# Performance work log

Hardware: AMD Instinct MI355X
Metric: run time of the kernel (lower is better)

## Reference

```python
import jax, jax.numpy as jnp
import numpy as np

N_HEADS = 32
N_KV_HEADS = 8
HEAD_DIM = 128  # hidden 4096 / 32
NEG_INF = -1e9


def _apply_rope(x, cos, sin):
    # x: [B, S, H, D]; cos/sin: [S, D//2] -> complex multiply on (even, odd) pairs
    B, S, H, D = x.shape
    xr = x.reshape(B, S, H, D // 2, 2)
    a, b = xr[..., 0], xr[..., 1]
    c = cos[None, :, None, :]
    s = sin[None, :, None, :]
    out = jnp.stack([a * c - b * s, a * s + b * c], axis=-1)
    return out.reshape(B, S, H, D)


def setup_inputs() -> dict:
    key = jax.random.key(0)
    ks = jax.random.split(key, 8)
    B, S, HID = 1, 2048, 4096
    hidden_states = jax.random.normal(ks[0], (B, S, HID), dtype=jnp.float32)
    # causal additive mask [1,1,S,S]
    causal = jnp.tril(jnp.ones((S, S), dtype=bool))
    attention_mask = jnp.where(causal, 0.0, NEG_INF).astype(jnp.float32)[None, None]
    # true rotary frequencies (theta=500000 as in llama3)
    half = HEAD_DIM // 2
    inv_freq = 1.0 / (500000.0 ** (np.arange(0, half, dtype=np.float32) / half))
    angles = np.arange(S, dtype=np.float32)[:, None] * inv_freq[None, :]
    freqs_cos = jnp.asarray(np.cos(angles), dtype=jnp.float32)
    freqs_sin = jnp.asarray(np.sin(angles), dtype=jnp.float32)
    sc = 0.02
    wq = jax.random.normal(ks[1], (HID, HID), dtype=jnp.float32) * sc
    wk = jax.random.normal(ks[2], (N_KV_HEADS * HEAD_DIM, HID), dtype=jnp.float32) * sc
    wv = jax.random.normal(ks[3], (N_KV_HEADS * HEAD_DIM, HID), dtype=jnp.float32) * sc
    wo = jax.random.normal(ks[4], (HID, HID), dtype=jnp.float32) * sc
    return {"hidden_states": hidden_states, "attention_mask": attention_mask,
            "freqs_cos": freqs_cos, "freqs_sin": freqs_sin,
            "wq": wq, "wk": wk, "wv": wv, "wo": wo}


def reference(hidden_states, attention_mask, freqs_cos, freqs_sin, wq, wk, wv, wo):
    B, S, HID = hidden_states.shape
    n_rep = N_HEADS // N_KV_HEADS
    # projections (torch Linear: x @ W.T)
    q = (hidden_states @ wq.T).reshape(B, S, N_HEADS, HEAD_DIM)
    k = (hidden_states @ wk.T).reshape(B, S, N_KV_HEADS, HEAD_DIM)
    v = (hidden_states @ wv.T).reshape(B, S, N_KV_HEADS, HEAD_DIM)
    # rotary on q (full cos/sin) and k
    q = _apply_rope(q, freqs_cos, freqs_sin)
    k = _apply_rope(k, freqs_cos, freqs_sin)
    # [B, H, S, D]
    q = q.transpose(0, 2, 1, 3)
    k = k.transpose(0, 2, 1, 3)
    v = v.transpose(0, 2, 1, 3)
    # GQA: repeat_interleave kv heads
    k = jnp.repeat(k, n_rep, axis=1)
    v = jnp.repeat(v, n_rep, axis=1)
    scores = jnp.einsum("bhqd,bhkd->bhqk", q, k) / jnp.sqrt(jnp.float32(HEAD_DIM))
    scores = scores + attention_mask
    probs = jax.nn.softmax(scores.astype(jnp.float32), axis=-1)
    attn = jnp.einsum("bhqk,bhkd->bhqd", probs, v)
    attn = attn.transpose(0, 2, 1, 3).reshape(B, S, N_HEADS * HEAD_DIM)
    return attn @ wo.T
```

## Files before the change

### kernel.cpp

```cpp
#include <hip/hip_runtime.h>
#include <hip/hip_bf16.h>
#include <math.h>

#define SEQ 2048
#define HID 4096
#define NH 32
#define NKV 8
#define HD 128
#define KVG (NH / NKV)
#define NQKV 6144

typedef __bf16 bf16x8 __attribute__((ext_vector_type(8)));
typedef float  f32x4  __attribute__((ext_vector_type(4)));

__device__ __forceinline__ unsigned short f2bf(float f) {
  union { float f; unsigned int u; } v; v.f = f;
  unsigned int r = v.u + 0x7FFFu + ((v.u >> 16) & 1u);
  return (unsigned short)(r >> 16);
}
__device__ __forceinline__ float bf2f(unsigned short h) {
  union { unsigned int u; float f; } v; v.u = ((unsigned int)h) << 16;
  return v.f;
}

__device__ __forceinline__ void glds16(const unsigned short* g, unsigned short* l) {
  __builtin_amdgcn_global_load_lds(
      (const __attribute__((address_space(1))) void*)g,
      (__attribute__((address_space(3))) void*)l, 16, 0, 0);
}

__global__ __launch_bounds__(256) void cvt_all(
    const float* __restrict__ H, const float* __restrict__ wq,
    const float* __restrict__ wk, const float* __restrict__ wv,
    const float* __restrict__ wo, unsigned short* __restrict__ ws)
{
  const long G1 = 1l << 20;
  const long M1 = 1l << 20;
  long g = (long)blockIdx.x * 256 + threadIdx.x;
  const float* src; unsigned short* dst; long rel;
  if      (g < 2 * G1) { src = H;  dst = ws;           rel = g;          }
  else if (g < 6 * G1) { src = wq; dst = ws + 8 * M1;  rel = g - 2 * G1; }
  else if (g < 7 * G1) { src = wk; dst = ws + 24 * M1; rel = g - 6 * G1; }
  else if (g < 8 * G1) { src = wv; dst = ws + 28 * M1; rel = g - 7 * G1; }
  else                 { src = wo; dst = ws + 32 * M1; rel = g - 8 * G1; }
  float4 v = ((const float4*)src)[rel];
  ushort4 o;
  o.x = f2bf(v.x); o.y = f2bf(v.y); o.z = f2bf(v.z); o.w = f2bf(v.w);
  ((ushort4*)dst)[rel] = o;
}

template<bool F32OUT>
__global__ __launch_bounds__(256) void gemm_nt(
    const unsigned short* __restrict__ A,
    const unsigned short* __restrict__ B,
    void* __restrict__ Cv,
    int M, int N, int K)
{
  __shared__ unsigned short As[128 * 64];
  __shared__ unsigned short Bs[128 * 64];
  const int t = threadIdx.x;
  const int lane = t & 63, wid = t >> 6;
  const int quad = lane >> 4, l16 = lane & 15;
  const int wm = (wid & 1) * 64, wn = (wid >> 1) * 64;
  const int m0 = blockIdx.y * 128, n0 = blockIdx.x * 128;

  int srow[4], sgch[4];
  const unsigned short* ga[4];
  const unsigned short* gb[4];
  unsigned short* la[4];
  unsigned short* lb[4];
  #pragma unroll
  for (int j = 0; j < 4; j++) {
    int pj = (wid * 4 + j) * 64 + lane;
    srow[j] = pj >> 3;
    sgch[j] = (pj & 7) ^ (srow[j] & 7);
    ga[j] = A + (size_t)(m0 + srow[j]) * K + sgch[j] * 8;
    gb[j] = B + (size_t)(n0 + srow[j]) * K + sgch[j] * 8;
    la[j] = &As[(wid * 4 + j) * 512];
    lb[j] = &Bs[(wid * 4 + j) * 512];
  }

  const f32x4 fzero = {0.f, 0.f, 0.f, 0.f};
  f32x4 acc[4][4];
  #pragma unroll
  for (int i = 0; i < 4; i++)
    #pragma unroll
    for (int j = 0; j < 4; j++) acc[i][j] = fzero;

  for (int k0 = 0; k0 < K; k0 += 64) {
    __syncthreads();
    #pragma unroll
    for (int j = 0; j < 4; j++) {
      glds16(ga[j], la[j]);
      glds16(gb[j], lb[j]);
      ga[j] += 64; gb[j] += 64;
    }
    __syncthreads();

    #pragma unroll
    for (int ks = 0; ks < 2; ks++) {
      bf16x8 af[4], bfr[4];
      #pragma unroll
      for (int mt = 0; mt < 4; mt++) {
        int row = wm + mt * 16 + l16;
        int cp = (ks * 4 + quad) ^ (l16 & 7);
        af[mt] = *(const bf16x8*)(&As[(row * 8 + cp) * 8]);
      }
      #pragma unroll
      for (int nt = 0; nt < 4; nt++) {
        int row = wn + nt * 16 + l16;
        int cp = (ks * 4 + quad) ^ (l16 & 7);
        bfr[nt] = *(const bf16x8*)(&Bs[(row * 8 + cp) * 8]);
      }
      #pragma unroll
      for (int mt = 0; mt < 4; mt++)
        #pragma unroll
        for (int nt = 0; nt < 4; nt++)
          acc[mt][nt] = __builtin_amdgcn_mfma_f32_16x16x32_bf16(af[mt], bfr[nt], acc[mt][nt], 0, 0, 0);
    }
  }

  #pragma unroll
  for (int mt = 0; mt < 4; mt++)
    #pragma unroll
    for (int nt = 0; nt < 4; nt++)
      #pragma unroll
      for (int r = 0; r < 4; r++) {
        int row = m0 + wm + mt * 16 + quad * 4 + r;
        int col = n0 + wn + nt * 16 + l16;
        float v = acc[mt][nt][r];
        if (F32OUT) ((float*)Cv)[(size_t)row * N + col] = v;
        else        ((unsigned short*)Cv)[(size_t)row * N + col] = f2bf(v);
      }
}

__global__ __launch_bounds__(256) void rope_vtrans(
    const unsigned short* __restrict__ QKVr,
    const float* __restrict__ cosT,
    const float* __restrict__ sinT,
    unsigned short* __restrict__ Qh,
    unsigned short* __restrict__ Kh,
    unsigned short* __restrict__ Vtg)
{
  __shared__ unsigned short T[64 * 66];
  int hh = blockIdx.y;
  int bx = blockIdx.x;
  int t = threadIdx.x;
  if (hh < NH + NKV) {
    int sub = t >> 6, d2 = t & 63;
    int s = bx * 4 + sub;
    float c = cosT[s * 64 + d2], sn = sinT[s * 64 + d2];
    const unsigned short* src;
    unsigned short* dst;
    if (hh < NH) {
      src = QKVr + (size_t)s * NQKV + hh * HD;
      dst = Qh + ((size_t)hh * SEQ + s) * HD;
    } else {
      int h = hh - NH;
      src = QKVr + (size_t)s * NQKV + HID + h * HD;
      dst = Kh + ((size_t)h * SEQ + s) * HD;
    }
    unsigned int u = *(const unsigned int*)(src + 2 * d2);
    float a = bf2f((unsigned short)(u & 0xffff)), b = bf2f((unsigned short)(u >> 16));
    unsigned int o = (unsigned int)f2bf(a * c - b * sn) | ((unsigned int)f2bf(a * sn + b * c) << 16);
    *(unsigned int*)(dst + 2 * d2) = o;
  } else {
    int idx = bx >> 5;
    int kvh = idx >> 1, d0 = (idx & 1) * 64;
    int s0 = (bx & 31) * 64;
    int si = t >> 2, dchunk = t & 3;
    const unsigned short* src = QKVr + (size_t)(s0 + si) * NQKV + HID + NKV * HD + kvh * HD + d0 + dchunk * 16;
    uint4 a = *(const uint4*)src;
    uint4 b = *(const uint4*)(src + 8);
    unsigned int va[8] = {a.x, a.y, a.z, a.w, b.x, b.y, b.z, b.w};
    #pragma unroll
    for (int j = 0; j < 8; j++)
      *(unsigned int*)(&T[si * 66 + dchunk * 16 + j * 2]) = va[j];
    __syncthreads();
    int di = t >> 2, schunk = t & 3;
    unsigned short px[16];
    #pragma unroll
    for (int j = 0; j < 16; j++) px[j] = T[(schunk * 16 + j) * 66 + di];
    unsigned short* dst = Vtg + ((size_t)kvh * HD + d0 + di) * SEQ + s0 + schunk * 16;
    *(uint4*)dst = *(uint4*)px;
    *(uint4*)(dst + 8) = *(uint4*)(px + 8);
  }
}

__global__ __launch_bounds__(256) void flash_kernel(
    const unsigned short* __restrict__ Qh,
    const unsigned short* __restrict__ Kh,
    const unsigned short* __restrict__ Vtg,
    unsigned short* __restrict__ Obf)
{
  __shared__ unsigned short Ks[64 * 128];
  __shared__ unsigned short Vs[128 * 64];
  __shared__ unsigned short Ps[4][32 * 72];

  const int h = blockIdx.y;
  const int pairp = blockIdx.x;
  const int kvh = h / KVG;
  const int t = threadIdx.x;
  const int lane = t & 63, w = t >> 6;
  const int quad = lane >> 4, l16 = lane & 15;
  const float scale = 0.08838834764831845f;
  const float SHIFT = 8.0f;

  bf16x8 ones;
  #pragma unroll
  for (int j = 0; j < 8; j++) ones[j] = (__bf16)1.0f;

  int krow[4], kgch[4], vrow[4], vgch[4];
  unsigned short* lk[4];
  unsigned short* lv[4];
  #pragma unroll
  for (int j = 0; j < 4; j++) {
    int pj = (w * 4 + j) * 64 + lane;
    krow[j] = pj >> 4; kgch[j] = (pj & 15) ^ (krow[j] & 15);
    vrow[j] = pj >> 3; vgch[j] = (pj & 7) ^ (vrow[j] & 7);
    lk[j] = &Ks[(w * 4 + j) * 512];
    lv[j] = &Vs[(w * 4 + j) * 512];
  }

  unsigned short* Pw = Ps[w];
  const f32x4 fzero = {0.f, 0.f, 0.f, 0.f};

  #pragma unroll
  for (int pass = 0; pass < 2; pass++) {
    const int qt = pass ? (15 - pairp) : pairp;
    const int q0 = qt * 128;
    const int qw = q0 + w * 32;

    bf16x8 aq[2][4];
    #pragma unroll
    for (int qg = 0; qg < 2; qg++) {
      const unsigned short* Qp = Qh + ((size_t)h * SEQ + qw + qg * 16 + l16) * HD;
      #pragma unroll
      for (int ks = 0; ks < 4; ks++) aq[qg][ks] = *(const bf16x8*)(Qp + ks * 32 + quad * 8);
    }

    f32x4 o[2][8];
    #pragma unroll
    for (int qg = 0; qg < 2; qg++)
      #pragma unroll
      for (int dt = 0; dt < 8; dt++) o[qg][dt] = fzero;
    f32x4 lacc[2] = {fzero, fzero};

    const unsigned short* gk[4];
    const unsigned short* gv[4];
    #pragma unroll
    for (int j = 0; j < 4; j++) {
      gk[j] = Kh + ((size_t)kvh * SEQ + krow[j]) * HD + kgch[j] * 8;
      gv[j] = Vtg + ((size_t)kvh * HD + vrow[j]) * SEQ + vgch[j] * 8;
    }

    for (int kv0 = 0; kv0 < q0 + 128; kv0 += 64) {
      __syncthreads();
      #pragma unroll
      for (int j = 0; j < 4; j++) {
        glds16(gk[j], lk[j]);
        glds16(gv[j], lv[j]);
        gk[j] += 64 * HD;
        gv[j] += 64;
      }
      __syncthreads();

      f32x4 sc[2][4];
      #pragma unroll
      for (int qg = 0; qg < 2; qg++)
        #pragma unroll
        for (int kvt = 0; kvt < 4; kvt++) sc[qg][kvt] = fzero;
      #pragma unroll
      for (int ks = 0; ks < 4; ks++)
        #pragma unroll
        for (int kvt = 0; kvt < 4; kvt++) {
          int row = kvt * 16 + l16;
          int cp = (ks * 4 + quad) ^ l16;
          bf16x8 bk = *(const bf16x8*)(&Ks[(row * 16 + cp) * 8]);
          sc[0][kvt] = __builtin_amdgcn_mfma_f32_16x16x32_bf16(bk, aq[0][ks], sc[0][kvt], 0, 0, 0);
          sc[1][kvt] = __builtin_amdgcn_mfma_f32_16x16x32_bf16(bk, aq[1][ks], sc[1][kvt], 0, 0, 0);
        }

      #pragma unroll
      for (int qg = 0; qg < 2; qg++) {
        int q = qw + qg * 16 + l16;
        #pragma unroll
        for (int kvt = 0; kvt < 4; kvt++) {
          unsigned short ph[4];
          #pragma unroll
          for (int r = 0; r < 4; r++) {
            int kv = kv0 + kvt * 16 + quad * 4 + r;
            float p = (kv > q) ? 0.f : __expf(fmaf(sc[qg][kvt][r], scale, -SHIFT));
            ph[r] = f2bf(p);
          }
          *(uint2*)(&Pw[(qg * 16 + l16) * 72 + kvt * 16 + quad * 4]) = *(const uint2*)ph;
        }
      }

      #pragma unroll
      for (int ks2 = 0; ks2 < 2; ks2++) {
        bf16x8 ap0 = *(const bf16x8*)(&Pw[(l16)      * 72 + ks2 * 32 + quad * 8]);
        bf16x8 ap1 = *(const bf16x8*)(&Pw[(16 + l16) * 72 + ks2 * 32 + quad * 8]);
        lacc[0] = __builtin_amdgcn_mfma_f32_16x16x32_bf16(ap0, ones, lacc[0], 0, 0, 0);
        lacc[1] = __builtin_amdgcn_mfma_f32_16x16x32_bf16(ap1, ones, lacc[1], 0, 0, 0);
        #pragma unroll
        for (int dt = 0; dt < 8; dt++) {
          int row = dt * 16 + l16;
          int cp = (ks2 * 4 + quad) ^ (l16 & 7);
          bf16x8 bv = *(const bf16x8*)(&Vs[(row * 8 + cp) * 8]);
          o[0][dt] = __builtin_amdgcn_mfma_f32_16x16x32_bf16(ap0, bv, o[0][dt], 0, 0, 0);
          o[1][dt] = __builtin_amdgcn_mfma_f32_16x16x32_bf16(ap1, bv, o[1][dt], 0, 0, 0);
        }
      }
    }

    #pragma unroll
    for (int qg = 0; qg < 2; qg++)
      #pragma unroll
      for (int dt = 0; dt < 8; dt++)
        #pragma unroll
        for (int r = 0; r < 4; r++) {
          int qq = qw + qg * 16 + quad * 4 + r;
          int d = dt * 16 + l16;
          Obf[(size_t)qq * HID + h * HD + d] = f2bf(o[qg][dt][r] / lacc[qg][r]);
        }
  }
}

extern "C" void kernel_launch(void* const* d_in, const int* in_sizes, int n_in,
                              void* d_out, int out_size, void* d_ws, size_t ws_size,
                              hipStream_t stream) {
  const float* H    = (const float*)d_in[0];
  const float* cosT = (const float*)d_in[2];
  const float* sinT = (const float*)d_in[3];
  const float* wq   = (const float*)d_in[4];
  const float* wk   = (const float*)d_in[5];
  const float* wv   = (const float*)d_in[6];
  const float* wo   = (const float*)d_in[7];

  unsigned short* ws = (unsigned short*)d_ws;
  const size_t M1 = 1u << 20;
  unsigned short* Hb   = ws;
  unsigned short* Wqkv = ws + (size_t)8  * M1;
  unsigned short* Wob  = ws + (size_t)32 * M1;
  unsigned short* QKVr = ws + (size_t)48 * M1;
  unsigned short* Qh   = ws + (size_t)8  * M1;
  unsigned short* Kh   = ws + (size_t)16 * M1;
  unsigned short* Vtg  = ws + (size_t)18 * M1;
  unsigned short* attn = ws;

  cvt_all<<<49152, 256, 0, stream>>>(H, wq, wk, wv, wo, ws);

  gemm_nt<false><<<dim3(48, 16), 256, 0, stream>>>(Hb, Wqkv, QKVr, SEQ, NQKV, HID);

  rope_vtrans<<<dim3(512, NH + NKV + 1), 256, 0, stream>>>(QKVr, cosT, sinT, Qh, Kh, Vtg);

  flash_kernel<<<dim3(8, NH), 256, 0, stream>>>(Qh, Kh, Vtg, attn);

  gemm_nt<true><<<dim3(32, 16), 256, 0, stream>>>(attn, Wob, d_out, SEQ, HID, HID);
}
```

Baseline: 490.4 us.

## Fuse RoPE and V transpose into QKV GEMM epilogue, split flash blocks

The QKV projection GEMM now applies rotary embedding in its epilogue, pairing even and odd columns with a lane shuffle, and writes V directly in transposed layout. This removes the separate rope_vtrans kernel and the intermediate QKV buffer round trip. The flash kernel launches one block per query tile instead of two passes per block, doubling the grid to 512 blocks for better occupancy and balance. The conversion kernel handles 8 floats per thread. The fused epilogue's scattered 2-byte stores, and the transposed V stores, may be less coalesced than the old dedicated kernel.

Measured after the change: 575.0 us. +17.2%, slower.

```diff
diff --git a/kernel.cpp b/kernel.cpp
--- a/kernel.cpp
+++ b/kernel.cpp
@@ -34,19 +34,23 @@
     const float* __restrict__ wk, const float* __restrict__ wv,
     const float* __restrict__ wo, unsigned short* __restrict__ ws)
 {
-  const long G1 = 1l << 20;
+  const long K512 = 524288;
   const long M1 = 1l << 20;
   long g = (long)blockIdx.x * 256 + threadIdx.x;
   const float* src; unsigned short* dst; long rel;
-  if      (g < 2 * G1) { src = H;  dst = ws;           rel = g;          }
-  else if (g < 6 * G1) { src = wq; dst = ws + 8 * M1;  rel = g - 2 * G1; }
-  else if (g < 7 * G1) { src = wk; dst = ws + 24 * M1; rel = g - 6 * G1; }
-  else if (g < 8 * G1) { src = wv; dst = ws + 28 * M1; rel = g - 7 * G1; }
-  else                 { src = wo; dst = ws + 32 * M1; rel = g - 8 * G1; }
-  float4 v = ((const float4*)src)[rel];
-  ushort4 o;
-  o.x = f2bf(v.x); o.y = f2bf(v.y); o.z = f2bf(v.z); o.w = f2bf(v.w);
-  ((ushort4*)dst)[rel] = o;
+  if      (g < 2 * K512) { src = H;  dst = ws;           rel = g;            }
+  else if (g < 6 * K512) { src = wq; dst = ws + 8 * M1;  rel = g - 2 * K512; }
+  else if (g < 7 * K512) { src = wk; dst = ws + 24 * M1; rel = g - 6 * K512; }
+  else if (g < 8 * K512) { src = wv; dst = ws + 28 * M1; rel = g - 7 * K512; }
+  else                   { src = wo; dst = ws + 32 * M1; rel = g - 8 * K512; }
+  float4 v0 = ((const float4*)src)[rel * 2];
+  float4 v1 = ((const float4*)src)[rel * 2 + 1];
+  uint4 o;
+  o.x = (unsigned)f2bf(v0.x) | ((unsigned)f2bf(v0.y) << 16);
+  o.y = (unsigned)f2bf(v0.z) | ((unsigned)f2bf(v0.w) << 16);
+  o.z = (unsigned)f2bf(v1.x) | ((unsigned)f2bf(v1.y) << 16);
+  o.w = (unsigned)f2bf(v1.z) | ((unsigned)f2bf(v1.w) << 16);
+  ((uint4*)dst)[rel] = o;
 }
 
 template<bool F32OUT>
@@ -64,7 +68,6 @@
   const int wm = (wid & 1) * 64, wn = (wid >> 1) * 64;
   const int m0 = blockIdx.y * 128, n0 = blockIdx.x * 128;
 
-  int srow[4], sgch[4];
   const unsigned short* ga[4];
   const unsigned short* gb[4];
   unsigned short* la[4];
@@ -72,10 +75,10 @@
   #pragma unroll
   for (int j = 0; j < 4; j++) {
     int pj = (wid * 4 + j) * 64 + lane;
-    srow[j] = pj >> 3;
-    sgch[j] = (pj & 7) ^ (srow[j] & 7);
-    ga[j] = A + (size_t)(m0 + srow[j]) * K + sgch[j] * 8;
-    gb[j] = B + (size_t)(n0 + srow[j]) * K + sgch[j] * 8;
+    int srow = pj >> 3;
+    int sgch = (pj & 7) ^ (srow & 7);
+    ga[j] = A + (size_t)(m0 + srow) * K + sgch * 8;
+    gb[j] = B + (size_t)(n0 + srow) * K + sgch * 8;
     la[j] = &As[(wid * 4 + j) * 512];
     lb[j] = &Bs[(wid * 4 + j) * 512];
   }
@@ -134,57 +137,108 @@
       }
 }
 
-__global__ __launch_bounds__(256) void rope_vtrans(
-    const unsigned short* __restrict__ QKVr,
+__global__ __launch_bounds__(256) void gemm_qkv(
+    const unsigned short* __restrict__ A,
+    const unsigned short* __restrict__ B,
     const float* __restrict__ cosT,
     const float* __restrict__ sinT,
     unsigned short* __restrict__ Qh,
     unsigned short* __restrict__ Kh,
     unsigned short* __restrict__ Vtg)
 {
-  __shared__ unsigned short T[64 * 66];
-  int hh = blockIdx.y;
-  int bx = blockIdx.x;
-  int t = threadIdx.x;
-  if (hh < NH + NKV) {
-    int sub = t >> 6, d2 = t & 63;
-    int s = bx * 4 + sub;
-    float c = cosT[s * 64 + d2], sn = sinT[s * 64 + d2];
-    const unsigned short* src;
-    unsigned short* dst;
-    if (hh < NH) {
-      src = QKVr + (size_t)s * NQKV + hh * HD;
-      dst = Qh + ((size_t)hh * SEQ + s) * HD;
-    } else {
-      int h = hh - NH;
-      src = QKVr + (size_t)s * NQKV + HID + h * HD;
-      dst = Kh + ((size_t)h * SEQ + s) * HD;
-    }
-    unsigned int u = *(const unsigned int*)(src + 2 * d2);
-    float a = bf2f((unsigned short)(u & 0xffff)), b = bf2f((unsigned short)(u >> 16));
-    unsigned int o = (unsigned int)f2bf(a * c - b * sn) | ((unsigned int)f2bf(a * sn + b * c) << 16);
-    *(unsigned int*)(dst + 2 * d2) = o;
-  } else {
-    int idx = bx >> 5;
-    int kvh = idx >> 1, d0 = (idx & 1) * 64;
-    int s0 = (bx & 31) * 64;
-    int si = t >> 2, dchunk = t & 3;
-    const unsigned short* src = QKVr + (size_t)(s0 + si) * NQKV + HID + NKV * HD + kvh * HD + d0 + dchunk * 16;
-    uint4 a = *(const uint4*)src;
-    uint4 b = *(const uint4*)(src + 8);
-    unsigned int va[8] = {a.x, a.y, a.z, a.w, b.x, b.y, b.z, b.w};
-    #pragma unroll
-    for (int j = 0; j < 8; j++)
-      *(unsigned int*)(&T[si * 66 + dchunk * 16 + j * 2]) = va[j];
-    __syncthreads();
-    int di = t >> 2, schunk = t & 3;
-    unsigned short px[16];
-    #pragma unroll
-    for (int j = 0; j < 16; j++) px[j] = T[(schunk * 16 + j) * 66 + di];
-    unsigned short* dst = Vtg + ((size_t)kvh * HD + d0 + di) * SEQ + s0 + schunk * 16;
-    *(uint4*)dst = *(uint4*)px;
-    *(uint4*)(dst + 8) = *(uint4*)(px + 8);
-  }
+  const int K = HID, N = NQKV;
+  __shared__ unsigned short As[128 * 64];
+  __shared__ unsigned short Bs[128 * 64];
+  const int t = threadIdx.x;
+  const int lane = t & 63, wid = t >> 6;
+  const int quad = lane >> 4, l16 = lane & 15;
+  const int wm = (wid & 1) * 64, wn = (wid >> 1) * 64;
+  const int m0 = blockIdx.y * 128, n0 = blockIdx.x * 128;
+
+  const unsigned short* ga[4];
+  const unsigned short* gb[4];
+  unsigned short* la[4];
+  unsigned short* lb[4];
+  #pragma unroll
+  for (int j = 0; j < 4; j++) {
+    int pj = (wid * 4 + j) * 64 + lane;
+    int srow = pj >> 3;
+    int sgch = (pj & 7) ^ (srow & 7);
+    ga[j] = A + (size_t)(m0 + srow) * K + sgch * 8;
+    gb[j] = B + (size_t)(n0 + srow) * K + sgch * 8;
+    la[j] = &As[(wid * 4 + j) * 512];
+    lb[j] = &Bs[(wid * 4 + j) * 512];
+  }
+
+  const f32x4 fzero = {0.f, 0.f, 0.f, 0.f};
+  f32x4 acc[4][4];
+  #pragma unroll
+  for (int i = 0; i < 4; i++)
+    #pragma unroll
+    for (int j = 0; j < 4; j++) acc[i][j] = fzero;
+
+  for (int k0 = 0; k0 < K; k0 += 64) {
+    __syncthreads();
+    #pragma unroll
+    for (int j = 0; j < 4; j++) {
+      glds16(ga[j], la[j]);
+      glds16(gb[j], lb[j]);
+      ga[j] += 64; gb[j] += 64;
+    }
+    __syncthreads();
+
+    #pragma unroll
+    for (int ks = 0; ks < 2; ks++) {
+      bf16x8 af[4], bfr[4];
+      #pragma unroll
+      for (int mt = 0; mt < 4; mt++) {
+        int row = wm + mt * 16 + l16;
+        int cp = (ks * 4 + quad) ^ (l16 & 7);
+        af[mt] = *(const bf16x8*)(&As[(row * 8 + cp) * 8]);
+      }
+      #pragma unroll
+      for (int nt = 0; nt < 4; nt++) {
+        int row = wn + nt * 16 + l16;
+        int cp = (ks * 4 + quad) ^ (l16 & 7);
+        bfr[nt] = *(const bf16x8*)(&Bs[(row * 8 + cp) * 8]);
+      }
+      #pragma unroll
+      for (int mt = 0; mt < 4; mt++)
+        #pragma unroll
+        for (int nt = 0; nt < 4; nt++)
+          acc[mt][nt] = __builtin_amdgcn_mfma_f32_16x16x32_bf16(af[mt], bfr[nt], acc[mt][nt], 0, 0, 0);
+    }
+  }
+
+  const float sgn = (l16 & 1) ? 1.f : -1.f;
+  #pragma unroll
+  for (int mt = 0; mt < 4; mt++)
+    #pragma unroll
+    for (int nt = 0; nt < 4; nt++) {
+      int col = n0 + wn + nt * 16 + l16;
+      int sbase = m0 + wm + mt * 16 + quad * 4;
+      if (col < HID + NKV * HD) {
+        int d = col & 127, d2 = d >> 1;
+        unsigned short* dst = (col < HID)
+            ? Qh + (size_t)(col >> 7) * SEQ * HD + d
+            : Kh + (size_t)((col - HID) >> 7) * SEQ * HD + d;
+        #pragma unroll
+        for (int r = 0; r < 4; r++) {
+          int s = sbase + r;
+          float own = acc[mt][nt][r];
+          float par = __shfl_xor(own, 1);
+          float c = cosT[s * 64 + d2], sn = sinT[s * 64 + d2];
+          dst[(size_t)s * HD] = f2bf(own * c + sgn * par * sn);
+        }
+      } else {
+        int cv = col - (HID + NKV * HD);
+        int kvh = cv >> 7, d = cv & 127;
+        unsigned short ph[4];
+        #pragma unroll
+        for (int r = 0; r < 4; r++) ph[r] = f2bf(acc[mt][nt][r]);
+        *(ushort4*)(Vtg + ((size_t)kvh * HD + d) * SEQ + sbase) = *(const ushort4*)ph;
+      }
+    }
 }
 
 __global__ __launch_bounds__(256) void flash_kernel(
@@ -197,8 +251,11 @@
   __shared__ unsigned short Vs[128 * 64];
   __shared__ unsigned short Ps[4][32 * 72];
 
-  const int h = blockIdx.y;
-  const int pairp = blockIdx.x;
+  const int lin = blockIdx.x + (blockIdx.y << 4);
+  const int idx = lin & 255, half = lin >> 8;
+  const int h = (idx >> 4) + half * 16;
+  const int qt = half ? (15 - (idx & 15)) : (idx & 15);
+  const int q0 = qt * 128;
   const int kvh = h / KVG;
   const int t = threadIdx.x;
   const int lane = t & 63, w = t >> 6;
@@ -210,121 +267,110 @@
   #pragma unroll
   for (int j = 0; j < 8; j++) ones[j] = (__bf16)1.0f;
 
-  int krow[4], kgch[4], vrow[4], vgch[4];
+  const unsigned short* gk[4];
+  const unsigned short* gv[4];
   unsigned short* lk[4];
   unsigned short* lv[4];
   #pragma unroll
   for (int j = 0; j < 4; j++) {
     int pj = (w * 4 + j) * 64 + lane;
-    krow[j] = pj >> 4; kgch[j] = (pj & 15) ^ (krow[j] & 15);
-    vrow[j] = pj >> 3; vgch[j] = (pj & 7) ^ (vrow[j] & 7);
+    int krow = pj >> 4, kgch = (pj & 15) ^ (krow & 15);
+    int vrow = pj >> 3, vgch = (pj & 7) ^ (vrow & 7);
+    gk[j] = Kh + ((size_t)kvh * SEQ + krow) * HD + kgch * 8;
+    gv[j] = Vtg + ((size_t)kvh * HD + vrow) * SEQ + vgch * 8;
     lk[j] = &Ks[(w * 4 + j) * 512];
     lv[j] = &Vs[(w * 4 + j) * 512];
   }
 
   unsigned short* Pw = Ps[w];
   const f32x4 fzero = {0.f, 0.f, 0.f, 0.f};
-
-  #pragma unroll
-  for (int pass = 0; pass < 2; pass++) {
-    const int qt = pass ? (15 - pairp) : pairp;
-    const int q0 = qt * 128;
-    const int qw = q0 + w * 32;
-
-    bf16x8 aq[2][4];
+  const int qw = q0 + w * 32;
+
+  bf16x8 aq[2][4];
+  #pragma unroll
+  for (int qg = 0; qg < 2; qg++) {
+    const unsigned short* Qp = Qh + ((size_t)h * SEQ + qw + qg * 16 + l16) * HD;
+    #pragma unroll
+    for (int ks = 0; ks < 4; ks++) aq[qg][ks] = *(const bf16x8*)(Qp + ks * 32 + quad * 8);
+  }
+
+  f32x4 o[2][8];
+  #pragma unroll
+  for (int qg = 0; qg < 2; qg++)
+    #pragma unroll
+    for (int dt = 0; dt < 8; dt++) o[qg][dt] = fzero;
+  f32x4 lacc[2] = {fzero, fzero};
+
+  for (int kv0 = 0; kv0 < q0 + 128; kv0 += 64) {
+    __syncthreads();
+    #pragma unroll
+    for (int j = 0; j < 4; j++) {
+      glds16(gk[j], lk[j]);
+      glds16(gv[j], lv[j]);
+      gk[j] += 64 * HD;
+      gv[j] += 64;
+    }
+    __syncthreads();
+
+    f32x4 sc[2][4];
+    #pragma unroll
+    for (int qg = 0; qg < 2; qg++)
+      #pragma unroll
+      for (int kvt = 0; kvt < 4; kvt++) sc[qg][kvt] = fzero;
+    #pragma unroll
+    for (int ks = 0; ks < 4; ks++)
+      #pragma unroll
+      for (int kvt = 0; kvt < 4; kvt++) {
+        int row = kvt * 16 + l16;
+        int cp = (ks * 4 + quad) ^ l16;
+        bf16x8 bk = *(const bf16x8*)(&Ks[(row * 16 + cp) * 8]);
+        sc[0][kvt] = __builtin_amdgcn_mfma_f32_16x16x32_bf16(bk, aq[0][ks], sc[0][kvt], 0, 0, 0);
+        sc[1][kvt] = __builtin_amdgcn_mfma_f32_16x16x32_bf16(bk, aq[1][ks], sc[1][kvt], 0, 0, 0);
+      }
+
     #pragma unroll
     for (int qg = 0; qg < 2; qg++) {
-      const unsigned short* Qp = Qh + ((size_t)h * SEQ + qw + qg * 16 + l16) * HD;
-      #pragma unroll
-      for (int ks = 0; ks < 4; ks++) aq[qg][ks] = *(const bf16x8*)(Qp + ks * 32 + quad * 8);
-    }
-
-    f32x4 o[2][8];
-    #pragma unroll
-    for (int qg = 0; qg < 2; qg++)
-      #pragma unroll
-      for (int dt = 0; dt < 8; dt++) o[qg][dt] = fzero;
-    f32x4 lacc[2] = {fzero, fzero};
-
-    const unsigned short* gk[4];
-    const unsigned short* gv[4];
-    #pragma unroll
-    for (int j = 0; j < 4; j++) {
-      gk[j] = Kh + ((size_t)kvh * SEQ + krow[j]) * HD + kgch[j] * 8;
-      gv[j] = Vtg + ((size_t)kvh * HD + vrow[j]) * SEQ + vgch[j] * 8;
-    }
-
-    for (int kv0 = 0; kv0 < q0 + 128; kv0 += 64) {
-      __syncthreads();
-      #pragma unroll
-      for (int j = 0; j < 4; j++) {
-        glds16(gk[j], lk[j]);
-        glds16(gv[j], lv[j]);
-        gk[j] += 64 * HD;
-        gv[j] += 64;
-      }
-      __syncthreads();
-
-      f32x4 sc[2][4];
-      #pragma unroll
-      for (int qg = 0; qg < 2; qg++)
-        #pragma unroll
-        for (int kvt = 0; kvt < 4; kvt++) sc[qg][kvt] = fzero;
-      #pragma unroll
-      for (int ks = 0; ks < 4; ks++)
-        #pragma unroll
-        for (int kvt = 0; kvt < 4; kvt++) {
-          int row = kvt * 16 + l16;
-          int cp = (ks * 4 + quad) ^ l16;
-          bf16x8 bk = *(const bf16x8*)(&Ks[(row * 16 + cp) * 8]);
-          sc[0][kvt] = __builtin_amdgcn_mfma_f32_16x16x32_bf16(bk, aq[0][ks], sc[0][kvt], 0, 0, 0);
-          sc[1][kvt] = __builtin_amdgcn_mfma_f32_16x16x32_bf16(bk, aq[1][ks], sc[1][kvt], 0, 0, 0);
-        }
-
-      #pragma unroll
-      for (int qg = 0; qg < 2; qg++) {
-        int q = qw + qg * 16 + l16;
-        #pragma unroll
-        for (int kvt = 0; kvt < 4; kvt++) {
-          unsigned short ph[4];
-          #pragma unroll
-          for (int r = 0; r < 4; r++) {
-            int kv = kv0 + kvt * 16 + quad * 4 + r;
-            float p = (kv > q) ? 0.f : __expf(fmaf(sc[qg][kvt][r], scale, -SHIFT));
-            ph[r] = f2bf(p);
-          }
-          *(uint2*)(&Pw[(qg * 16 + l16) * 72 + kvt * 16 + quad * 4]) = *(const uint2*)ph;
-        }
-      }
-
-      #pragma unroll
-      for (int ks2 = 0; ks2 < 2; ks2++) {
-        bf16x8 ap0 = *(const bf16x8*)(&Pw[(l16)      * 72 + ks2 * 32 + quad * 8]);
-        bf16x8 ap1 = *(const bf16x8*)(&Pw[(16 + l16) * 72 + ks2 * 32 + quad * 8]);
-        lacc[0] = __builtin_amdgcn_mfma_f32_16x16x32_bf16(ap0, ones, lacc[0], 0, 0, 0);
-        lacc[1] = __builtin_amdgcn_mfma_f32_16x16x32_bf16(ap1, ones, lacc[1], 0, 0, 0);
-        #pragma unroll
-        for (int dt = 0; dt < 8; dt++) {
-          int row = dt * 16 + l16;
-          int cp = (ks2 * 4 + quad) ^ (l16 & 7);
-          bf16x8 bv = *(const bf16x8*)(&Vs[(row * 8 + cp) * 8]);
-          o[0][dt] = __builtin_amdgcn_mfma_f32_16x16x32_bf16(ap0, bv, o[0][dt], 0, 0, 0);
-          o[1][dt] = __builtin_amdgcn_mfma_f32_16x16x32_bf16(ap1, bv, o[1][dt], 0, 0, 0);
-        }
-      }
-    }
-
-    #pragma unroll
-    for (int qg = 0; qg < 2; qg++)
-      #pragma unroll
-      for (int dt = 0; dt < 8; dt++)
+      int q = qw + qg * 16 + l16;
+      #pragma unroll
+      for (int kvt = 0; kvt < 4; kvt++) {
+        unsigned short ph[4];
         #pragma unroll
         for (int r = 0; r < 4; r++) {
-          int qq = qw + qg * 16 + quad * 4 + r;
-          int d = dt * 16 + l16;
-          Obf[(size_t)qq * HID + h * HD + d] = f2bf(o[qg][dt][r] / lacc[qg][r]);
+          int kv = kv0 + kvt * 16 + quad * 4 + r;
+          float p = (kv > q) ? 0.f : __expf(fmaf(sc[qg][kvt][r], scale, -SHIFT));
+          ph[r] = f2bf(p);
         }
-  }
+        *(uint2*)(&Pw[(qg * 16 + l16) * 72 + kvt * 16 + quad * 4]) = *(const uint2*)ph;
+      }
+    }
+
+    #pragma unroll
+    for (int ks2 = 0; ks2 < 2; ks2++) {
+      bf16x8 ap0 = *(const bf16x8*)(&Pw[(l16)      * 72 + ks2 * 32 + quad * 8]);
+      bf16x8 ap1 = *(const bf16x8*)(&Pw[(16 + l16) * 72 + ks2 * 32 + quad * 8]);
+      lacc[0] = __builtin_amdgcn_mfma_f32_16x16x32_bf16(ap0, ones, lacc[0], 0, 0, 0);
+      lacc[1] = __builtin_amdgcn_mfma_f32_16x16x32_bf16(ap1, ones, lacc[1], 0, 0, 0);
+      #pragma unroll
+      for (int dt = 0; dt < 8; dt++) {
+        int row = dt * 16 + l16;
+        int cp = (ks2 * 4 + quad) ^ (l16 & 7);
+        bf16x8 bv = *(const bf16x8*)(&Vs[(row * 8 + cp) * 8]);
+        o[0][dt] = __builtin_amdgcn_mfma_f32_16x16x32_bf16(ap0, bv, o[0][dt], 0, 0, 0);
+        o[1][dt] = __builtin_amdgcn_mfma_f32_16x16x32_bf16(ap1, bv, o[1][dt], 0, 0, 0);
+      }
+    }
+  }
+
+  #pragma unroll
+  for (int qg = 0; qg < 2; qg++)
+    #pragma unroll
+    for (int dt = 0; dt < 8; dt++)
+      #pragma unroll
+      for (int r = 0; r < 4; r++) {
+        int qq = qw + qg * 16 + quad * 4 + r;
+        int d = dt * 16 + l16;
+        Obf[(size_t)qq * HID + h * HD + d] = f2bf(o[qg][dt][r] / lacc[qg][r]);
+      }
 }
 
 extern "C" void kernel_launch(void* const* d_in, const int* in_sizes, int n_in,
@@ -343,19 +389,16 @@
   unsigned short* Hb   = ws;
   unsigned short* Wqkv = ws + (size_t)8  * M1;
   unsigned short* Wob  = ws + (size_t)32 * M1;
-  unsigned short* QKVr = ws + (size_t)48 * M1;
-  unsigned short* Qh   = ws + (size_t)8  * M1;
-  unsigned short* Kh   = ws + (size_t)16 * M1;
-  unsigned short* Vtg  = ws + (size_t)18 * M1;
+  unsigned short* Qh   = ws + (size_t)48 * M1;
+  unsigned short* Kh   = ws + (size_t)56 * M1;
+  unsigned short* Vtg  = ws + (size_t)58 * M1;
   unsigned short* attn = ws;
 
-  cvt_all<<<49152, 256, 0, stream>>>(H, wq, wk, wv, wo, ws);
-
-  gemm_nt<false><<<dim3(48, 16), 256, 0, stream>>>(Hb, Wqkv, QKVr, SEQ, NQKV, HID);
-
-  rope_vtrans<<<dim3(512, NH + NKV + 1), 256, 0, stream>>>(QKVr, cosT, sinT, Qh, Kh, Vtg);
-
-  flash_kernel<<<dim3(8, NH), 256, 0, stream>>>(Qh, Kh, Vtg, attn);
+  cvt_all<<<24576, 256, 0, stream>>>(H, wq, wk, wv, wo, ws);
+
+  gemm_qkv<<<dim3(48, 16), 256, 0, stream>>>(Hb, Wqkv, cosT, sinT, Qh, Kh, Vtg);
+
+  flash_kernel<<<dim3(16, 32), 256, 0, stream>>>(Qh, Kh, Vtg, attn);
 
   gemm_nt<true><<<dim3(32, 16), 256, 0, stream>>>(attn, Wob, d_out, SEQ, HID, HID);
 }
```
